# Kernel optimization log

Hardware: AMD Instinct MI355X
Metric: run time of the kernel (lower is better)

Reference implementation:

```python
import jax, jax.numpy as jnp
import numpy as np

EPS = 1.0 / 137.0
OUT_FEATURES = 8192

def setup_inputs() -> dict:
    key = jax.random.key(0)
    k1, k2 = jax.random.split(key)
    x = jax.random.normal(k1, (8, 2048, 2048), dtype=jnp.float32)
    # lecun_normal-like scale for kernel
    kernel = jax.random.normal(k2, (2048, OUT_FEATURES), dtype=jnp.float32) * (1.0 / np.sqrt(2048))
    bias = jnp.zeros((OUT_FEATURES,), dtype=jnp.float32)
    alpha = jnp.ones((1,), dtype=jnp.float32)
    return {"x": x, "kernel": kernel, "bias": bias, "alpha": alpha}

def reference(x, kernel, bias, alpha):
    # y = x @ kernel : [B, S, out]
    y = jnp.einsum("bsd,do->bso", x, kernel)
    x_sq = jnp.sum(x * x, axis=-1, keepdims=True)            # [B, S, 1]
    k_sq = jnp.sum(kernel * kernel, axis=0, keepdims=True)   # [1, out]
    distances = x_sq + k_sq - 2.0 * y                         # ||x - w||^2
    y = (y * y) / (distances + EPS)
    y = y + bias.reshape((1,) * (y.ndim - 1) + (-1,))
    scale = (jnp.sqrt(jnp.float32(OUT_FEATURES)) / jnp.log1p(jnp.float32(OUT_FEATURES))) ** alpha
    return y * scale
```

## Files before the change

kernel.cpp:

```cpp
#include <hip/hip_runtime.h>
#include <hip/hip_bf16.h>
#include <math.h>


#define EPS_F (1.0f / 137.0f)
#define M_DIM 16384
#define N_DIM 8192
#define K_DIM 2048

typedef __attribute__((ext_vector_type(8))) short short8;
typedef __attribute__((ext_vector_type(4))) float f32x4;

__device__ __forceinline__ unsigned short f2bf(float f) {
  unsigned int u = __float_as_uint(f);
  u += 0x7fffu + ((u >> 16) & 1u);
  return (unsigned short)(u >> 16);
}

typedef __attribute__((address_space(1))) const unsigned int as1_cuint;
typedef __attribute__((address_space(3))) unsigned int as3_uint;

__device__ __forceinline__ void gload16(const void* g, void* lds_wave_base) {
  __builtin_amdgcn_global_load_lds((as1_cuint*)g, (as3_uint*)lds_wave_base, 16, 0, 0);
}


__global__ __launch_bounds__(256) void k_conv_x(const float* __restrict__ x,
                                                unsigned short* __restrict__ xbf,
                                                float* __restrict__ xs) {
  const int row = blockIdx.x;
  const int t = threadIdx.x;
  const float4* xr = (const float4*)(x + (size_t)row * K_DIM);
  ushort4* orow = (ushort4*)(xbf + (size_t)row * K_DIM);
  float s = 0.f;
#pragma unroll
  for (int i = 0; i < 2; ++i) {
    float4 v = xr[t + i * 256];
    s += v.x * v.x + v.y * v.y + v.z * v.z + v.w * v.w;
    ushort4 o;
    o.x = f2bf(v.x); o.y = f2bf(v.y); o.z = f2bf(v.z); o.w = f2bf(v.w);
    orow[t + i * 256] = o;
  }
#pragma unroll
  for (int off = 32; off > 0; off >>= 1) s += __shfl_down(s, off, 64);
  __shared__ float red[4];
  if ((t & 63) == 0) red[t >> 6] = s;
  __syncthreads();
  if (t == 0) xs[row] = red[0] + red[1] + red[2] + red[3];
}

__global__ __launch_bounds__(256) void k_conv_kT(const float* __restrict__ w,
                                                 unsigned short* __restrict__ bt) {
  __shared__ float tile[32][33];
  const int tx = threadIdx.x;
  const int ty = threadIdx.y;
  const int n0 = blockIdx.x * 32;
  const int k0 = blockIdx.y * 32;
#pragma unroll
  for (int j = 0; j < 32; j += 8)
    tile[ty + j][tx] = w[(size_t)(k0 + ty + j) * N_DIM + n0 + tx];
  __syncthreads();
#pragma unroll
  for (int j = 0; j < 32; j += 8)
    bt[(size_t)(n0 + ty + j) * K_DIM + k0 + tx] = f2bf(tile[tx][ty + j]);
}

__global__ __launch_bounds__(256) void k_ksq_part(const float* __restrict__ w,
                                                  float* __restrict__ kpart) {
  const int col = blockIdx.x * 256 + threadIdx.x;
  const int kb = blockIdx.y;
  float s = 0.f;
#pragma unroll 4
  for (int k = kb * 128; k < kb * 128 + 128; ++k) {
    float v = w[(size_t)k * N_DIM + col];
    s += v * v;
  }
  kpart[kb * N_DIM + col] = s;
}

__global__ __launch_bounds__(256) void k_ksq_fin(const float* __restrict__ kpart,
                                                 float* __restrict__ ks) {
  const int col = blockIdx.x * 256 + threadIdx.x;
  float s = 0.f;
#pragma unroll
  for (int kb = 0; kb < 16; ++kb) s += kpart[kb * N_DIM + col];
  ks[col] = s;
}


#define MFMA_OP(d, va, vb) \
  d = __builtin_amdgcn_mfma_f32_16x16x32_bf16(va, vb, d, 0, 0, 0)

#define FENCE asm volatile("" ::: "memory")
#define BAR do { FENCE; __builtin_amdgcn_s_barrier(); FENCE; } while (0)
#define VMCNT8 asm volatile("s_waitcnt vmcnt(8)" ::: "memory")

__global__ __launch_bounds__(512) void k_gemm(const unsigned short* __restrict__ A,
                                              const unsigned short* __restrict__ B,
                                              const float* __restrict__ xs,
                                              const float* __restrict__ ks,
                                              const float* __restrict__ bias,
                                              const float* __restrict__ alpha,
                                              float* __restrict__ out) {
  __shared__ __align__(16) char lds[131072];
  char* sA = lds;
  char* sB = lds + 65536;

  const int t = threadIdx.x;
  const int lane = t & 63;
  const int wid = t >> 6;
  const int wr = wid >> 2;
  const int wc = wid & 3;
  const int lr = lane & 15;
  const int kh = lane >> 4;
  const int swz = (lr & 7) << 4;

  const int bid = blockIdx.x;
  const int xcd = bid & 7;
  const int sub = bid >> 3;
  const int c   = sub >> 5;
  const int tm = ((xcd >> 1) << 4) + ((c >> 1) << 2) + ((sub >> 3) & 3);
  const int tn = ((xcd & 1) << 4) + ((c & 1) << 3) + (sub & 7);
  const size_t rowM0 = (size_t)tm * 256;
  const size_t colN0 = (size_t)tn * 256;

  const int l8 = lane >> 3;
  const int col16 = (lane & 7) ^ (l8 & 7);
  const int rA_base = (wid < 4) ? wid * 8 : 128 + (wid - 4) * 8;
  const unsigned short* gA0 = A + (rowM0 + rA_base + l8) * K_DIM + col16 * 8;
  const unsigned short* gB0 = B + (colN0 + wid * 8 + l8) * K_DIM + col16 * 8;

#define STAGE_A(b, s, ko) \
  gload16(gA0 + (size_t)(s) * 32 * K_DIM + (ko), \
          sA + (b) * 32768 + (rA_base + (s) * 32) * 128)
#define STAGE_B(b, j, ko) \
  gload16(gB0 + (size_t)(j) * 64 * K_DIM + (ko), \
          sB + (b) * 32768 + ((j) * 64 + wid * 8) * 128)

#define RD_A(b, m, kk) \
  (*(const short8*)(sA + (b) * 32768 + (wr * 128 + (m) * 16 + lr) * 128 + \
                    (((kk) * 64 + kh * 16) ^ swz)))
#define RD_B(b, n, kk) \
  (*(const short8*)(sB + (b) * 32768 + (wc * 64 + (n) * 16 + lr) * 128 + \
                    (((kk) * 64 + kh * 16) ^ swz)))

  f32x4 acc[8][4] = {};
  short8 a00, a01, a10, a11;
  short8 b0[4], b1[4];

#define MFMA16(mb) do { \
  __builtin_amdgcn_s_setprio(1); \
  MFMA_OP(acc[mb][0], a00, b0[0]); MFMA_OP(acc[mb][1], a00, b0[1]); \
  MFMA_OP(acc[mb][2], a00, b0[2]); MFMA_OP(acc[mb][3], a00, b0[3]); \
  MFMA_OP(acc[(mb)+1][0], a10, b0[0]); MFMA_OP(acc[(mb)+1][1], a10, b0[1]); \
  MFMA_OP(acc[(mb)+1][2], a10, b0[2]); MFMA_OP(acc[(mb)+1][3], a10, b0[3]); \
  MFMA_OP(acc[mb][0], a01, b1[0]); MFMA_OP(acc[mb][1], a01, b1[1]); \
  MFMA_OP(acc[mb][2], a01, b1[2]); MFMA_OP(acc[mb][3], a01, b1[3]); \
  MFMA_OP(acc[(mb)+1][0], a11, b1[0]); MFMA_OP(acc[(mb)+1][1], a11, b1[1]); \
  MFMA_OP(acc[(mb)+1][2], a11, b1[2]); MFMA_OP(acc[(mb)+1][3], a11, b1[3]); \
  __builtin_amdgcn_s_setprio(0); \
} while (0)

#define PHASE_FIRST(b) do { \
  VMCNT8; BAR; \
  b0[0] = RD_B(b, 0, 0); b0[1] = RD_B(b, 1, 0); b0[2] = RD_B(b, 2, 0); b0[3] = RD_B(b, 3, 0); \
  b1[0] = RD_B(b, 0, 1); b1[1] = RD_B(b, 1, 1); b1[2] = RD_B(b, 2, 1); b1[3] = RD_B(b, 3, 1); \
  a00 = RD_A(b, 0, 0); a01 = RD_A(b, 0, 1); a10 = RD_A(b, 1, 0); a11 = RD_A(b, 1, 1); \
  MFMA16(0); \
  BAR; \
} while (0)

#define PHASE_REST(b, mb, STG) do { \
  a00 = RD_A(b, mb, 0); a01 = RD_A(b, mb, 1); \
  a10 = RD_A(b, (mb)+1, 0); a11 = RD_A(b, (mb)+1, 1); \
  STG; \
  BAR; \
  MFMA16(mb); \
  BAR; \
} while (0)

  STAGE_A(0, 0, 0); STAGE_B(0, 0, 0);
  STAGE_A(0, 1, 0); STAGE_B(0, 1, 0);
  STAGE_A(0, 2, 0); STAGE_B(0, 2, 0);
  STAGE_A(0, 3, 0); STAGE_B(0, 3, 0);
  STAGE_A(1, 0, 64); STAGE_B(1, 0, 64);
  STAGE_A(1, 1, 64); STAGE_B(1, 1, 64);
  STAGE_A(1, 2, 64); STAGE_B(1, 2, 64);

#pragma unroll 1
  for (int it = 0; it < 16; ++it) {
    const int kT1 = it * 128 + 64;
    const int kS0 = (it < 15) ? it * 128 + 128 : 0;
    const int kS1 = (it < 15) ? it * 128 + 192 : 0;
    STAGE_A(1, 3, kT1); STAGE_B(1, 3, kT1);
    PHASE_FIRST(0);
    PHASE_REST(0, 2, (STAGE_A(0, 0, kS0), STAGE_B(0, 0, kS0)));
    PHASE_REST(0, 4, (STAGE_A(0, 1, kS0), STAGE_B(0, 1, kS0)));
    PHASE_REST(0, 6, (STAGE_A(0, 2, kS0), STAGE_B(0, 2, kS0)));
    STAGE_A(0, 3, kS0); STAGE_B(0, 3, kS0);
    PHASE_FIRST(1);
    PHASE_REST(1, 2, (STAGE_A(1, 0, kS1), STAGE_B(1, 0, kS1)));
    PHASE_REST(1, 4, (STAGE_A(1, 1, kS1), STAGE_B(1, 1, kS1)));
    PHASE_REST(1, 6, (STAGE_A(1, 2, kS1), STAGE_B(1, 2, kS1)));
  }

  asm volatile("s_waitcnt vmcnt(0)" ::: "memory");

  const float scale = powf(sqrtf(8192.0f) / log1pf(8192.0f), alpha[0]);
#pragma unroll
  for (int m = 0; m < 8; ++m) {
#pragma unroll
    for (int r = 0; r < 4; ++r) {
      const size_t grow = rowM0 + wr * 128 + m * 16 + kh * 4 + r;
      const float xq = xs[grow];
      float* orow = out + grow * N_DIM;
#pragma unroll
      for (int n = 0; n < 4; ++n) {
        const int gcol = (int)colN0 + wc * 64 + n * 16 + lr;
        const float y = acc[m][n][r];
        const float d = xq + ks[gcol] - 2.0f * y + EPS_F;
        const float v = y * y * __builtin_amdgcn_rcpf(d);
        orow[gcol] = (v + bias[gcol]) * scale;
      }
    }
  }
}


extern "C" void kernel_launch(void* const* d_in, const int* in_sizes, int n_in,
                              void* d_out, int out_size, void* d_ws, size_t ws_size,
                              hipStream_t stream) {
  const float* x     = (const float*)d_in[0];
  const float* w     = (const float*)d_in[1];
  const float* bias  = (const float*)d_in[2];
  const float* alpha = (const float*)d_in[3];
  float* out = (float*)d_out;
  char* ws = (char*)d_ws;

  unsigned short* xbf = (unsigned short*)(ws);
  unsigned short* ktb = (unsigned short*)(ws + 67108864);
  float* xs    = (float*)(ws + 100663296);
  float* ks    = (float*)(ws + 100728832);
  float* kpart = (float*)(ws + 100761600);

  k_conv_x<<<M_DIM, 256, 0, stream>>>(x, xbf, xs);
  k_conv_kT<<<dim3(N_DIM / 32, K_DIM / 32), dim3(32, 8), 0, stream>>>(w, ktb);
  k_ksq_part<<<dim3(N_DIM / 256, 16), 256, 0, stream>>>(w, kpart);
  k_ksq_fin<<<N_DIM / 256, 256, 0, stream>>>(kpart, ks);
  k_gemm<<<(M_DIM / 256) * (N_DIM / 256), 512, 0, stream>>>(xbf, ktb, xs, ks, bias, alpha, out);
}
```

Measured before the change: 573.7 us.

## Double-buffer LDS fragment registers in GEMM and fuse kernel-norm into transpose

The GEMM main loop now ping-pongs two sets of A-fragment registers and two sets of B-fragment registers. The next phase's LDS reads are issued before the barrier and MFMA block of the current phase, which hides LDS read latency behind matrix math. The vmcnt waits are retuned to the new staging order, and launch_bounds now requests two blocks per CU. Separately, the column sum-of-squares of the weight is computed inside the transpose/convert kernel, which removes a separate pass over the weight matrix. The costs are higher register pressure and a dependency on the workspace being large enough for 64 partial rows.

```diff
diff --git a/kernel.cpp b/kernel.cpp
--- a/kernel.cpp
+++ b/kernel.cpp
@@ -47,6 +47,35 @@
   if ((t & 63) == 0) red[t >> 6] = s;
   __syncthreads();
   if (t == 0) xs[row] = red[0] + red[1] + red[2] + red[3];
+}
+
+__global__ __launch_bounds__(256) void k_conv_kT_fused(const float* __restrict__ w,
+                                                       unsigned short* __restrict__ bt,
+                                                       float* __restrict__ kpart) {
+  __shared__ float tile[32][33];
+  __shared__ float psum[8][33];
+  const int tx = threadIdx.x;
+  const int ty = threadIdx.y;
+  const int n0 = blockIdx.x * 32;
+  const int k0 = blockIdx.y * 32;
+  float ss = 0.f;
+#pragma unroll
+  for (int j = 0; j < 32; j += 8) {
+    float v = w[(size_t)(k0 + ty + j) * N_DIM + n0 + tx];
+    tile[ty + j][tx] = v;
+    ss += v * v;
+  }
+  psum[ty][tx] = ss;
+  __syncthreads();
+#pragma unroll
+  for (int j = 0; j < 32; j += 8)
+    bt[(size_t)(n0 + ty + j) * K_DIM + k0 + tx] = f2bf(tile[tx][ty + j]);
+  if (ty == 0) {
+    float s = 0.f;
+#pragma unroll
+    for (int r = 0; r < 8; ++r) s += psum[r][tx];
+    kpart[(size_t)(k0 >> 5) * N_DIM + n0 + tx] = s;
+  }
 }
 
 __global__ __launch_bounds__(256) void k_conv_kT(const float* __restrict__ w,
@@ -79,11 +108,10 @@
 }
 
 __global__ __launch_bounds__(256) void k_ksq_fin(const float* __restrict__ kpart,
-                                                 float* __restrict__ ks) {
+                                                 float* __restrict__ ks, int nkb) {
   const int col = blockIdx.x * 256 + threadIdx.x;
   float s = 0.f;
-#pragma unroll
-  for (int kb = 0; kb < 16; ++kb) s += kpart[kb * N_DIM + col];
+  for (int kb = 0; kb < nkb; ++kb) s += kpart[(size_t)kb * N_DIM + col];
   ks[col] = s;
 }
 
@@ -93,15 +121,16 @@
 
 #define FENCE asm volatile("" ::: "memory")
 #define BAR do { FENCE; __builtin_amdgcn_s_barrier(); FENCE; } while (0)
-#define VMCNT8 asm volatile("s_waitcnt vmcnt(8)" ::: "memory")
-
-__global__ __launch_bounds__(512) void k_gemm(const unsigned short* __restrict__ A,
-                                              const unsigned short* __restrict__ B,
-                                              const float* __restrict__ xs,
-                                              const float* __restrict__ ks,
-                                              const float* __restrict__ bias,
-                                              const float* __restrict__ alpha,
-                                              float* __restrict__ out) {
+#define VMCNT4 asm volatile("s_waitcnt vmcnt(4)" ::: "memory")
+#define VMCNT6 asm volatile("s_waitcnt vmcnt(6)" ::: "memory")
+
+__global__ __launch_bounds__(512, 2) void k_gemm(const unsigned short* __restrict__ A,
+                                                 const unsigned short* __restrict__ B,
+                                                 const float* __restrict__ xs,
+                                                 const float* __restrict__ ks,
+                                                 const float* __restrict__ bias,
+                                                 const float* __restrict__ alpha,
+                                                 float* __restrict__ out) {
   __shared__ __align__(16) char lds[131072];
   char* sA = lds;
   char* sB = lds + 65536;
@@ -145,38 +174,29 @@
                     (((kk) * 64 + kh * 16) ^ swz)))
 
   f32x4 acc[8][4] = {};
-  short8 a00, a01, a10, a11;
-  short8 b0[4], b1[4];
-
-#define MFMA16(mb) do { \
+  short8 aX0, aX1, aX2, aX3, aY0, aY1, aY2, aY3;
+  short8 bX[8], bY[8];
+
+#define LOAD_A(AS, b, mb) do { \
+  AS##0 = RD_A(b, mb, 0); AS##1 = RD_A(b, mb, 1); \
+  AS##2 = RD_A(b, (mb)+1, 0); AS##3 = RD_A(b, (mb)+1, 1); \
+} while (0)
+#define LOAD_B(BS, b) do { \
+  BS[0] = RD_B(b, 0, 0); BS[1] = RD_B(b, 1, 0); BS[2] = RD_B(b, 2, 0); BS[3] = RD_B(b, 3, 0); \
+  BS[4] = RD_B(b, 0, 1); BS[5] = RD_B(b, 1, 1); BS[6] = RD_B(b, 2, 1); BS[7] = RD_B(b, 3, 1); \
+} while (0)
+
+#define MFMA16(mb, AS, BS) do { \
   __builtin_amdgcn_s_setprio(1); \
-  MFMA_OP(acc[mb][0], a00, b0[0]); MFMA_OP(acc[mb][1], a00, b0[1]); \
-  MFMA_OP(acc[mb][2], a00, b0[2]); MFMA_OP(acc[mb][3], a00, b0[3]); \
-  MFMA_OP(acc[(mb)+1][0], a10, b0[0]); MFMA_OP(acc[(mb)+1][1], a10, b0[1]); \
-  MFMA_OP(acc[(mb)+1][2], a10, b0[2]); MFMA_OP(acc[(mb)+1][3], a10, b0[3]); \
-  MFMA_OP(acc[mb][0], a01, b1[0]); MFMA_OP(acc[mb][1], a01, b1[1]); \
-  MFMA_OP(acc[mb][2], a01, b1[2]); MFMA_OP(acc[mb][3], a01, b1[3]); \
-  MFMA_OP(acc[(mb)+1][0], a11, b1[0]); MFMA_OP(acc[(mb)+1][1], a11, b1[1]); \
-  MFMA_OP(acc[(mb)+1][2], a11, b1[2]); MFMA_OP(acc[(mb)+1][3], a11, b1[3]); \
+  MFMA_OP(acc[mb][0], AS##0, BS[0]); MFMA_OP(acc[mb][1], AS##0, BS[1]); \
+  MFMA_OP(acc[mb][2], AS##0, BS[2]); MFMA_OP(acc[mb][3], AS##0, BS[3]); \
+  MFMA_OP(acc[(mb)+1][0], AS##2, BS[0]); MFMA_OP(acc[(mb)+1][1], AS##2, BS[1]); \
+  MFMA_OP(acc[(mb)+1][2], AS##2, BS[2]); MFMA_OP(acc[(mb)+1][3], AS##2, BS[3]); \
+  MFMA_OP(acc[mb][0], AS##1, BS[4]); MFMA_OP(acc[mb][1], AS##1, BS[5]); \
+  MFMA_OP(acc[mb][2], AS##1, BS[6]); MFMA_OP(acc[mb][3], AS##1, BS[7]); \
+  MFMA_OP(acc[(mb)+1][0], AS##3, BS[4]); MFMA_OP(acc[(mb)+1][1], AS##3, BS[5]); \
+  MFMA_OP(acc[(mb)+1][2], AS##3, BS[6]); MFMA_OP(acc[(mb)+1][3], AS##3, BS[7]); \
   __builtin_amdgcn_s_setprio(0); \
-} while (0)
-
-#define PHASE_FIRST(b) do { \
-  VMCNT8; BAR; \
-  b0[0] = RD_B(b, 0, 0); b0[1] = RD_B(b, 1, 0); b0[2] = RD_B(b, 2, 0); b0[3] = RD_B(b, 3, 0); \
-  b1[0] = RD_B(b, 0, 1); b1[1] = RD_B(b, 1, 1); b1[2] = RD_B(b, 2, 1); b1[3] = RD_B(b, 3, 1); \
-  a00 = RD_A(b, 0, 0); a01 = RD_A(b, 0, 1); a10 = RD_A(b, 1, 0); a11 = RD_A(b, 1, 1); \
-  MFMA16(0); \
-  BAR; \
-} while (0)
-
-#define PHASE_REST(b, mb, STG) do { \
-  a00 = RD_A(b, mb, 0); a01 = RD_A(b, mb, 1); \
-  a10 = RD_A(b, (mb)+1, 0); a11 = RD_A(b, (mb)+1, 1); \
-  STG; \
-  BAR; \
-  MFMA16(mb); \
-  BAR; \
 } while (0)
 
   STAGE_A(0, 0, 0); STAGE_B(0, 0, 0);
@@ -186,22 +206,32 @@
   STAGE_A(1, 0, 64); STAGE_B(1, 0, 64);
   STAGE_A(1, 1, 64); STAGE_B(1, 1, 64);
   STAGE_A(1, 2, 64); STAGE_B(1, 2, 64);
+  VMCNT6;
+  BAR;
+  LOAD_B(bX, 0);
+  LOAD_A(aX, 0, 0);
 
 #pragma unroll 1
   for (int it = 0; it < 16; ++it) {
     const int kT1 = it * 128 + 64;
     const int kS0 = (it < 15) ? it * 128 + 128 : 0;
     const int kS1 = (it < 15) ? it * 128 + 192 : 0;
-    STAGE_A(1, 3, kT1); STAGE_B(1, 3, kT1);
-    PHASE_FIRST(0);
-    PHASE_REST(0, 2, (STAGE_A(0, 0, kS0), STAGE_B(0, 0, kS0)));
-    PHASE_REST(0, 4, (STAGE_A(0, 1, kS0), STAGE_B(0, 1, kS0)));
-    PHASE_REST(0, 6, (STAGE_A(0, 2, kS0), STAGE_B(0, 2, kS0)));
-    STAGE_A(0, 3, kS0); STAGE_B(0, 3, kS0);
-    PHASE_FIRST(1);
-    PHASE_REST(1, 2, (STAGE_A(1, 0, kS1), STAGE_B(1, 0, kS1)));
-    PHASE_REST(1, 4, (STAGE_A(1, 1, kS1), STAGE_B(1, 1, kS1)));
-    PHASE_REST(1, 6, (STAGE_A(1, 2, kS1), STAGE_B(1, 2, kS1)));
+    LOAD_A(aY, 0, 2); STAGE_A(1, 3, kT1); STAGE_B(1, 3, kT1);
+    BAR; MFMA16(0, aX, bX); BAR;
+    LOAD_A(aX, 0, 4); STAGE_A(0, 0, kS0); STAGE_B(0, 0, kS0);
+    BAR; MFMA16(2, aY, bX); BAR;
+    LOAD_A(aY, 0, 6); STAGE_A(0, 1, kS0); STAGE_B(0, 1, kS0);
+    BAR; MFMA16(4, aX, bX); VMCNT4; BAR;
+    LOAD_B(bY, 1); LOAD_A(aX, 1, 0); STAGE_A(0, 2, kS0); STAGE_B(0, 2, kS0);
+    BAR; MFMA16(6, aY, bX); BAR;
+    LOAD_A(aY, 1, 2); STAGE_A(0, 3, kS0); STAGE_B(0, 3, kS0);
+    BAR; MFMA16(0, aX, bY); BAR;
+    LOAD_A(aX, 1, 4); STAGE_A(1, 0, kS1); STAGE_B(1, 0, kS1);
+    BAR; MFMA16(2, aY, bY); BAR;
+    LOAD_A(aY, 1, 6); STAGE_A(1, 1, kS1); STAGE_B(1, 1, kS1);
+    BAR; MFMA16(4, aX, bY); VMCNT4; BAR;
+    LOAD_B(bX, 0); LOAD_A(aX, 0, 0); STAGE_A(1, 2, kS1); STAGE_B(1, 2, kS1);
+    BAR; MFMA16(6, aY, bY); BAR;
   }
 
   asm volatile("s_waitcnt vmcnt(0)" ::: "memory");
@@ -244,8 +274,13 @@
   float* kpart = (float*)(ws + 100761600);
 
   k_conv_x<<<M_DIM, 256, 0, stream>>>(x, xbf, xs);
-  k_conv_kT<<<dim3(N_DIM / 32, K_DIM / 32), dim3(32, 8), 0, stream>>>(w, ktb);
-  k_ksq_part<<<dim3(N_DIM / 256, 16), 256, 0, stream>>>(w, kpart);
-  k_ksq_fin<<<N_DIM / 256, 256, 0, stream>>>(kpart, ks);
+  if (ws_size >= 100761600ull + (size_t)64 * N_DIM * 4) {
+    k_conv_kT_fused<<<dim3(N_DIM / 32, K_DIM / 32), dim3(32, 8), 0, stream>>>(w, ktb, kpart);
+    k_ksq_fin<<<N_DIM / 256, 256, 0, stream>>>(kpart, ks, 64);
+  } else {
+    k_conv_kT<<<dim3(N_DIM / 32, K_DIM / 32), dim3(32, 8), 0, stream>>>(w, ktb);
+    k_ksq_part<<<dim3(N_DIM / 256, 16), 256, 0, stream>>>(w, kpart);
+    k_ksq_fin<<<N_DIM / 256, 256, 0, stream>>>(kpart, ks, 16);
+  }
   k_gemm<<<(M_DIM / 256) * (N_DIM / 256), 512, 0, stream>>>(xbf, ktb, xs, ks, bias, alpha, out);
 }
```

Measured after the change: 960.8 us. 1.67x slower.
